# Optimization experiments

Measured on AMD Instinct MI355X. Metric: run time of the kernel, lower is better.

The kernel has to match this reference:

```python
import jax, jax.numpy as jnp
import numpy as np

EMBED_DIM = 1024
NUM_HEADS = 16
HEAD_DIM = EMBED_DIM // NUM_HEADS
ROPE_BASE = 10000.0


def setup_inputs() -> dict:
    key = jax.random.key(0)
    ks = jax.random.split(key, 9)
    B, S, E = 2, 2048, EMBED_DIM
    scale = 1.0 / np.sqrt(E)
    x = jax.random.normal(ks[0], (B, S, E), dtype=jnp.float32)
    Wq = jax.random.normal(ks[1], (E, E), dtype=jnp.float32) * scale
    bq = jnp.zeros((E,), dtype=jnp.float32)
    Wk = jax.random.normal(ks[2], (E, E), dtype=jnp.float32) * scale
    bk = jnp.zeros((E,), dtype=jnp.float32)
    Wv = jax.random.normal(ks[3], (E, E), dtype=jnp.float32) * scale
    bv = jnp.zeros((E,), dtype=jnp.float32)
    Wo = jax.random.normal(ks[4], (E, E), dtype=jnp.float32) * scale
    bo = jnp.zeros((E,), dtype=jnp.float32)
    return {"x": x, "Wq": Wq, "bq": bq, "Wk": Wk, "bk": bk,
            "Wv": Wv, "bv": bv, "Wo": Wo, "bo": bo}


def _rotary_emb(seq_len, dtype=jnp.float32):
    half = HEAD_DIM // 2
    inv_freq = 1.0 / (ROPE_BASE ** (jnp.arange(half, dtype=dtype) / half))
    pos = jnp.arange(seq_len, dtype=dtype)
    sinusoid = pos[:, None] * inv_freq[None, :]  # [S, half]
    sin = jnp.sin(sinusoid)
    cos = jnp.cos(sinusoid)
    # interleave-duplicate: (s0,s0,s1,s1,...) -> [S, HEAD_DIM]
    sin = jnp.stack((sin, sin), axis=-1).reshape(seq_len, HEAD_DIM)
    cos = jnp.stack((cos, cos), axis=-1).reshape(seq_len, HEAD_DIM)
    return sin, cos


def _rotate_half(x):
    x1 = x[..., ::2]
    x2 = x[..., 1::2]
    return jnp.stack((-x2, x1), axis=-1).reshape(x.shape)


def _apply_rope(x, sin, cos):
    # x: [B, H, S, D]; sin/cos: [S, D]
    return x * cos[None, None] + _rotate_half(x) * sin[None, None]


def reference(x, Wq, bq, Wk, bk, Wv, bv, Wo, bo):
    B, S, E = x.shape
    H, D = NUM_HEADS, HEAD_DIM

    def proj(W, b):
        t = x @ W.T + b  # [B, S, E]
        return t.reshape(B, S, H, D).transpose(0, 2, 1, 3)  # [B, H, S, D]

    q = proj(Wq, bq)
    k = proj(Wk, bk)
    v = proj(Wv, bv)

    sin, cos = _rotary_emb(S, x.dtype)
    q = _apply_rope(q, sin, cos)
    k = _apply_rope(k, sin, cos)

    scores = jnp.einsum("bhqd,bhkd->bhqk", q, k) / jnp.sqrt(jnp.asarray(D, x.dtype))
    causal = jnp.tril(jnp.ones((S, S), dtype=bool))  # keep lower triangle
    scores = jnp.where(causal[None, None], scores, -jnp.inf)
    weights = jax.nn.softmax(scores, axis=-1)
    out = jnp.einsum("bhqk,bhkd->bhqd", weights, v)
    out = out.transpose(0, 2, 1, 3).reshape(B, S, E)
    return out @ Wo.T + bo
```

## Files before the change

### kernel.cpp

```cpp
#include <hip/hip_runtime.h>
#include <hip/hip_bf16.h>
#include <cstdint>
#include <cstddef>

typedef __hip_bfloat16 bf16;
typedef __attribute__((ext_vector_type(8))) short bf16x8;
typedef __attribute__((ext_vector_type(4))) float f32x4;

#define AS1C(p) ((const __attribute__((address_space(1))) void*)(p))
#define AS3(p)  ((__attribute__((address_space(3))) void*)(p))

constexpr int B_ = 2, S_ = 2048, E_ = 1024, H_ = 16, D_ = 64;
constexpr int M_ = B_ * S_;
constexpr float QSCALE_ = 0.125f * 1.44269504088896340736f;

__device__ __forceinline__ void gload_lds16(const bf16* g, bf16* l) {
  __builtin_amdgcn_global_load_lds(AS1C(g), AS3(l), 16, 0, 0);
}

__device__ __forceinline__ void cast4(const float* __restrict__ in, bf16* __restrict__ out, int i) {
  float4 v = reinterpret_cast<const float4*>(in)[i];
  union { bf16 b[4]; short4 s; } u;
  u.b[0] = __float2bfloat16(v.x);
  u.b[1] = __float2bfloat16(v.y);
  u.b[2] = __float2bfloat16(v.z);
  u.b[3] = __float2bfloat16(v.w);
  reinterpret_cast<short4*>(out)[i] = u.s;
}

__global__ void prep_kernel(const float* __restrict__ x,
                            const float* __restrict__ Wq, const float* __restrict__ Wk,
                            const float* __restrict__ Wv, const float* __restrict__ Wo,
                            const float* __restrict__ bq, const float* __restrict__ bk,
                            const float* __restrict__ bv,
                            bf16* __restrict__ xb, bf16* __restrict__ Wqkvb,
                            bf16* __restrict__ Wob, float* __restrict__ bqkv,
                            float* __restrict__ sintab, float* __restrict__ costab) {
  const int b = blockIdx.x, t = threadIdx.x;
  if (b < 4096) {
    cast4(x, xb, b * 256 + t);
  } else if (b < 5120) {
    cast4(Wo, Wob, (b - 4096) * 256 + t);
  } else if (b < 8192) {
    const int i = (b - 5120) * 256 + t;
    const int which = i >> 18;
    const int j = i & ((1 << 18) - 1);
    const float* src = which == 0 ? Wq : (which == 1 ? Wk : Wv);
    cast4(src, Wqkvb + (size_t)which * E_ * E_, j);
  } else if (b < 8448) {
    const int idx = (b - 8192) * 256 + t;
    const int s = idx >> 5, i = idx & 31;
    float inv = powf(10000.0f, -(float)i / 32.0f);
    float ang = (float)s * inv;
    sintab[idx] = sinf(ang);
    costab[idx] = cosf(ang);
  } else {
    for (int j = t; j < 768; j += 256) {
      const int which = j >> 8, jj = j & 255;
      const float* src = which == 0 ? bq : (which == 1 ? bk : bv);
      reinterpret_cast<float4*>(bqkv)[j] = reinterpret_cast<const float4*>(src)[jj];
    }
  }
}

__global__ __launch_bounds__(256)
void gemm_qkv(const bf16* __restrict__ A, const bf16* __restrict__ W,
              const float* __restrict__ bias,
              bf16* __restrict__ Qo, bf16* __restrict__ Ko, bf16* __restrict__ Vo,
              const float* __restrict__ sintab, const float* __restrict__ costab)
{
  constexpr int K = 1024, BK = 32;
  __shared__ __align__(16) bf16 smem[128 * 136];
  bf16* As = smem;
  bf16* Bs = smem + 128 * 32;
  const int tid = threadIdx.x;
  const int lane = tid & 63, wid = tid >> 6;
  const int g = lane >> 4, r16 = lane & 15;
  const int wr = wid >> 1, wc = wid & 1;

  const int nwg = gridDim.x * gridDim.y;
  const int flat = blockIdx.y * gridDim.x + blockIdx.x;
  const int cpx = nwg >> 3;
  const int f2 = (flat & 7) * cpx + (flat >> 3);
  const int m0 = (f2 / gridDim.x) * 128, n0 = (f2 % gridDim.x) * 128;

  const f32x4 fz = {0.f, 0.f, 0.f, 0.f};
  f32x4 acc[4][4];
#pragma unroll
  for (int mi = 0; mi < 4; ++mi)
#pragma unroll
    for (int ni = 0; ni < 4; ++ni) acc[mi][ni] = fz;

  const bf16* Abase = A + (size_t)m0 * K;
  const bf16* Wbase = W + (size_t)n0 * K;
  const int c0 = tid, c1 = 256 + tid;

  for (int k0 = 0; k0 < K; k0 += BK) {
    __syncthreads();
    gload_lds16(Abase + (size_t)(c0 >> 2) * K + k0 + (c0 & 3) * 8, As + c0 * 8);
    gload_lds16(Abase + (size_t)(c1 >> 2) * K + k0 + (c1 & 3) * 8, As + c1 * 8);
    gload_lds16(Wbase + (size_t)(c0 >> 2) * K + k0 + (c0 & 3) * 8, Bs + c0 * 8);
    gload_lds16(Wbase + (size_t)(c1 >> 2) * K + k0 + (c1 & 3) * 8, Bs + c1 * 8);
    __syncthreads();

    bf16x8 af[4], bfr[4];
#pragma unroll
    for (int mi = 0; mi < 4; ++mi)
      af[mi] = *reinterpret_cast<const bf16x8*>(As + (wr * 64 + mi * 16 + r16) * BK + 8 * g);
#pragma unroll
    for (int ni = 0; ni < 4; ++ni)
      bfr[ni] = *reinterpret_cast<const bf16x8*>(Bs + (wc * 64 + ni * 16 + r16) * BK + 8 * g);
    __builtin_amdgcn_s_setprio(1);
#pragma unroll
    for (int mi = 0; mi < 4; ++mi)
#pragma unroll
      for (int ni = 0; ni < 4; ++ni)
        acc[mi][ni] = __builtin_amdgcn_mfma_f32_16x16x32_bf16(af[mi], bfr[ni], acc[mi][ni], 0, 0, 0);
    __builtin_amdgcn_s_setprio(0);
  }

  const int b = m0 >> 11;
  if (n0 >= 2048) {
    __syncthreads();
#pragma unroll
    for (int mi = 0; mi < 4; ++mi) {
#pragma unroll
      for (int ni = 0; ni < 4; ++ni) {
        const int n_local = wc * 64 + ni * 16 + r16;
        const float bv = bias[n0 + n_local];
        const int m_base = wr * 64 + mi * 16 + g * 4;
        union { bf16 b4[4]; short4 s4; } u;
#pragma unroll
        for (int r = 0; r < 4; ++r) u.b4[r] = __float2bfloat16(acc[mi][ni][r] + bv);
        *reinterpret_cast<short4*>(&smem[n_local * 136 + m_base]) = u.s4;
      }
    }
    __syncthreads();
    const int srow0 = m0 & (S_ - 1);
#pragma unroll
    for (int i = 0; i < 8; ++i) {
      const int c = i * 256 + tid;
      const int row = c >> 4, cc = c & 15;
      const bf16x8 v = *reinterpret_cast<const bf16x8*>(&smem[row * 136 + cc * 8]);
      const int n = n0 + row;
      const int h = (n >> 6) & 15, d = n & 63;
      *reinterpret_cast<bf16x8*>(&Vo[((size_t)(b * H_ + h) * D_ + d) * S_ + srow0 + cc * 8]) = v;
    }
  } else {
#pragma unroll
    for (int mi = 0; mi < 4; ++mi) {
#pragma unroll
      for (int ni = 0; ni < 4; ++ni) {
        const int gn = n0 + wc * 64 + ni * 16 + r16;
        const float bv = bias[gn];
#pragma unroll
        for (int r = 0; r < 4; ++r) {
          const int gm = m0 + wr * 64 + mi * 16 + g * 4 + r;
          float val = acc[mi][ni][r] + bv;
          const int d = gn & 63;
          const int srow = gm & (S_ - 1);
          const float cs = costab[srow * 32 + (d >> 1)];
          const float sn = sintab[srow * 32 + (d >> 1)];
          const float pv = __shfl_xor(val, 1);
          val = (d & 1) ? (val * cs + pv * sn) : (val * cs - pv * sn);
          const int h = (gn >> 6) & 15;
          const size_t bh = (size_t)(b * H_ + h);
          if (gn < 1024) {
            Qo[(bh * S_ + srow) * D_ + d] = __float2bfloat16(val * QSCALE_);
          } else {
            Ko[(bh * S_ + srow) * D_ + d] = __float2bfloat16(val);
          }
        }
      }
    }
  }
}

__global__ __launch_bounds__(256)
void gemm_o(const bf16* __restrict__ A, const bf16* __restrict__ W,
            const float* __restrict__ bias, float* __restrict__ outF)
{
  constexpr int K = 1024, BK = 32;
  __shared__ __align__(16) bf16 As[64 * BK];
  __shared__ __align__(16) bf16 Bs[128 * BK];
  const int tid = threadIdx.x;
  const int lane = tid & 63;
  const int wc = tid >> 6;
  const int g = lane >> 4, r16 = lane & 15;

  const int flat = blockIdx.x;
  const int f2 = (flat & 7) * 64 + (flat >> 3);
  const int m0 = (f2 >> 3) * 64, n0 = (f2 & 7) * 128;

  const f32x4 fz = {0.f, 0.f, 0.f, 0.f};
  f32x4 acc[4][2];
#pragma unroll
  for (int mi = 0; mi < 4; ++mi)
#pragma unroll
    for (int ni = 0; ni < 2; ++ni) acc[mi][ni] = fz;

  const bf16* Abase = A + (size_t)m0 * K;
  const bf16* Wbase = W + (size_t)n0 * K;
  const int c0 = tid, c1 = 256 + tid;

  for (int k0 = 0; k0 < K; k0 += BK) {
    __syncthreads();
    gload_lds16(Abase + (size_t)(c0 >> 2) * K + k0 + (c0 & 3) * 8, As + c0 * 8);
    gload_lds16(Wbase + (size_t)(c0 >> 2) * K + k0 + (c0 & 3) * 8, Bs + c0 * 8);
    gload_lds16(Wbase + (size_t)(c1 >> 2) * K + k0 + (c1 & 3) * 8, Bs + c1 * 8);
    __syncthreads();

    bf16x8 af[4], bfr[2];
#pragma unroll
    for (int mi = 0; mi < 4; ++mi)
      af[mi] = *reinterpret_cast<const bf16x8*>(As + (mi * 16 + r16) * BK + 8 * g);
#pragma unroll
    for (int ni = 0; ni < 2; ++ni)
      bfr[ni] = *reinterpret_cast<const bf16x8*>(Bs + (wc * 32 + ni * 16 + r16) * BK + 8 * g);
    __builtin_amdgcn_s_setprio(1);
#pragma unroll
    for (int mi = 0; mi < 4; ++mi)
#pragma unroll
      for (int ni = 0; ni < 2; ++ni)
        acc[mi][ni] = __builtin_amdgcn_mfma_f32_16x16x32_bf16(af[mi], bfr[ni], acc[mi][ni], 0, 0, 0);
    __builtin_amdgcn_s_setprio(0);
  }

#pragma unroll
  for (int mi = 0; mi < 4; ++mi)
#pragma unroll
    for (int ni = 0; ni < 2; ++ni) {
      const int gn = n0 + wc * 32 + ni * 16 + r16;
      const float bv = bias[gn];
#pragma unroll
      for (int r = 0; r < 4; ++r) {
        const int gm = m0 + mi * 16 + g * 4 + r;
        outF[(size_t)gm * 1024 + gn] = acc[mi][ni][r] + bv;
      }
    }
}

__global__ __launch_bounds__(256, 4)
void attn_kernel(const bf16* __restrict__ Q, const bf16* __restrict__ Kg,
                 const bf16* __restrict__ Vtg, bf16* __restrict__ Og)
{
  __shared__ __align__(16) bf16 Ks[2][64 * 64];
  __shared__ __align__(16) bf16 Vs[2][64 * 64];
  const int flat = blockIdx.x;
  const int bh = flat & 31;
  const int qblk = 31 - (flat >> 5);
  const int tid = threadIdx.x, lane = tid & 63, wid = tid >> 6;
  const int g = lane >> 4, r16 = lane & 15;
  const bf16* Qb = Q + (size_t)bh * S_ * D_;
  const bf16* Kb = Kg + (size_t)bh * S_ * D_;
  const bf16* Vb = Vtg + (size_t)bh * D_ * S_;
  const int b = bh >> 4, h = bh & 15;
  bf16* Ob = Og + (size_t)b * S_ * E_ + h * D_;

  const int q0 = qblk * 64;
  const int qw0 = q0 + wid * 16;
  const int nkt = qblk + 1;
  const f32x4 fz = {0.f, 0.f, 0.f, 0.f};

  bf16x8 qf[2];
#pragma unroll
  for (int hh = 0; hh < 2; ++hh)
    qf[hh] = *reinterpret_cast<const bf16x8*>(Qb + (size_t)(qw0 + r16) * 64 + hh * 32 + 8 * g);

  f32x4 oacc[4];
#pragma unroll
  for (int dt = 0; dt < 4; ++dt) oacc[dt] = fz;
  float mrow = -__builtin_inff();
  float lrow = 0.f;

  const int kc0 = tid, kc1 = 256 + tid;
  const int glsrc = (g << 4) + (g << 2);

  auto stage = [&](const bf16* srcbase, size_t rowstride, bf16* dst) {
    const int r0 = kc0 >> 3, cc0 = kc0 & 7;
    gload_lds16(srcbase + (size_t)r0 * rowstride + ((cc0 ^ (r0 & 7)) * 8), dst + kc0 * 8);
    const int r1 = kc1 >> 3, cc1 = kc1 & 7;
    gload_lds16(srcbase + (size_t)r1 * rowstride + ((cc1 ^ (r1 & 7)) * 8), dst + kc1 * 8);
  };

  stage(Kb, 64, Ks[0]);
  stage(Vb, S_, Vs[0]);
  __syncthreads();
  int cur = 0;

  for (int kt = 0; kt < nkt; ++kt) {
    const int k0 = kt * 64;
    if (kt + 1 < nkt) {
      stage(Kb + (size_t)(k0 + 64) * 64, 64, Ks[cur ^ 1]);
      stage(Vb + (k0 + 64), S_, Vs[cur ^ 1]);
    }

    if (k0 <= qw0 + 15) {
      const bf16* ksp = Ks[cur];
      const bf16* vsp = Vs[cur];
      const int sw = r16 & 7;
      f32x4 ps[4];
      __builtin_amdgcn_s_setprio(1);
#pragma unroll
      for (int kf = 0; kf < 4; ++kf) {
        const int krow = kf * 16 + r16;
        const bf16x8 ka = *reinterpret_cast<const bf16x8*>(&ksp[krow * 64 + ((g ^ sw) * 8)]);
        const bf16x8 kb = *reinterpret_cast<const bf16x8*>(&ksp[krow * 64 + (((g + 4) ^ sw) * 8)]);
        f32x4 sa = __builtin_amdgcn_mfma_f32_16x16x32_bf16(ka, qf[0], fz, 0, 0, 0);
        ps[kf] = __builtin_amdgcn_mfma_f32_16x16x32_bf16(kb, qf[1], sa, 0, 0, 0);
      }
      __builtin_amdgcn_s_setprio(0);
      if (k0 + 63 > qw0) {
        const int qmk = qw0 + r16 - k0;
#pragma unroll
        for (int kf = 0; kf < 4; ++kf)
#pragma unroll
          for (int r = 0; r < 4; ++r)
            if (kf * 16 + 4 * g + r > qmk) ps[kf][r] = -1e30f;
      }
      float tm = fmaxf(fmaxf(ps[0][0], ps[0][1]), fmaxf(ps[0][2], ps[0][3]));
#pragma unroll
      for (int kf = 1; kf < 4; ++kf)
        tm = fmaxf(tm, fmaxf(fmaxf(ps[kf][0], ps[kf][1]), fmaxf(ps[kf][2], ps[kf][3])));
      tm = fmaxf(tm, __shfl_xor(tm, 16));
      tm = fmaxf(tm, __shfl_xor(tm, 32));
      if (__any((tm - mrow > 8.f) ? 1 : 0)) {
        const float mn = fmaxf(mrow, tm);
        const float scl = exp2f(mrow - mn);
        mrow = mn;
        lrow *= scl;
        float sclo[4];
#pragma unroll
        for (int r = 0; r < 4; ++r) sclo[r] = __shfl(scl, glsrc + r);
#pragma unroll
        for (int dt = 0; dt < 4; ++dt)
#pragma unroll
          for (int r = 0; r < 4; ++r) oacc[dt][r] *= sclo[r];
      }
      float ssum = 0.f;
#pragma unroll
      for (int kf = 0; kf < 4; ++kf)
#pragma unroll
        for (int r = 0; r < 4; ++r) {
          const float p = exp2f(ps[kf][r] - mrow);
          ps[kf][r] = p;
          ssum += p;
        }
      lrow += ssum;
      unsigned int pk[4][2];
#pragma unroll
      for (int kf = 0; kf < 4; ++kf)
#pragma unroll
        for (int w = 0; w < 2; ++w) {
          unsigned int rr;
          asm("v_cvt_pk_bf16_f32 %0, %1, %2" : "=v"(rr) : "v"(ps[kf][2 * w]), "v"(ps[kf][2 * w + 1]));
          pk[kf][w] = rr;
        }
      const int srcA = ((g & 1) << 5) + r16;
      const bool ghi = g >= 2;
#pragma unroll
      for (int ks = 0; ks < 2; ++ks) {
        const unsigned int a0 = (unsigned)__shfl((int)pk[2 * ks][0], srcA);
        const unsigned int b0 = (unsigned)__shfl((int)pk[2 * ks + 1][0], srcA);
        const unsigned int a1 = (unsigned)__shfl((int)pk[2 * ks][1], srcA);
        const unsigned int b1 = (unsigned)__shfl((int)pk[2 * ks + 1][1], srcA);
        const unsigned int a2 = (unsigned)__shfl((int)pk[2 * ks][0], srcA + 16);
        const unsigned int b2 = (unsigned)__shfl((int)pk[2 * ks + 1][0], srcA + 16);
        const unsigned int a3 = (unsigned)__shfl((int)pk[2 * ks][1], srcA + 16);
        const unsigned int b3 = (unsigned)__shfl((int)pk[2 * ks + 1][1], srcA + 16);
        union { unsigned int w[4]; bf16x8 v; } aw;
        aw.w[0] = ghi ? b0 : a0;
        aw.w[1] = ghi ? b1 : a1;
        aw.w[2] = ghi ? b2 : a2;
        aw.w[3] = ghi ? b3 : a3;
        __builtin_amdgcn_s_setprio(1);
#pragma unroll
        for (int dt = 0; dt < 4; ++dt) {
          const int d = dt * 16 + r16;
          const bf16x8 vf = *reinterpret_cast<const bf16x8*>(
              &vsp[d * 64 + (((ks * 4 + g) ^ (r16 & 7)) * 8)]);
          oacc[dt] = __builtin_amdgcn_mfma_f32_16x16x32_bf16(aw.v, vf, oacc[dt], 0, 0, 0);
        }
        __builtin_amdgcn_s_setprio(0);
      }
    }

    __syncthreads();
    cur ^= 1;
  }

  float s = lrow;
  s += __shfl_xor(s, 16);
  s += __shfl_xor(s, 32);
  const float linv = 1.0f / s;
  float linvo[4];
#pragma unroll
  for (int r = 0; r < 4; ++r) linvo[r] = __shfl(linv, glsrc + r);
#pragma unroll
  for (int dt = 0; dt < 4; ++dt)
#pragma unroll
    for (int r = 0; r < 4; ++r) {
      const int qrow = qw0 + g * 4 + r;
      Ob[(size_t)qrow * E_ + dt * 16 + r16] = __float2bfloat16(oacc[dt][r] * linvo[r]);
    }
}

extern "C" void kernel_launch(void* const* d_in, const int* in_sizes, int n_in,
                              void* d_out, int out_size, void* d_ws, size_t ws_size,
                              hipStream_t stream) {
  const float* x  = (const float*)d_in[0];
  const float* Wq = (const float*)d_in[1];
  const float* bq = (const float*)d_in[2];
  const float* Wk = (const float*)d_in[3];
  const float* bk = (const float*)d_in[4];
  const float* Wv = (const float*)d_in[5];
  const float* bv = (const float*)d_in[6];
  const float* Wo = (const float*)d_in[7];
  const float* bo = (const float*)d_in[8];
  float* out = (float*)d_out;

  char* ws = (char*)d_ws;
  size_t off = 0;
  auto alloc = [&](size_t bytes) -> char* {
    char* p = ws + off; off += (bytes + 255) & ~(size_t)255; return p;
  };
  bf16* xb    = (bf16*)alloc((size_t)M_ * E_ * 2);
  bf16* Wqkvb = (bf16*)alloc((size_t)3 * E_ * E_ * 2);
  bf16* Wob   = (bf16*)alloc((size_t)E_ * E_ * 2);
  float* bqkv = (float*)alloc((size_t)3 * E_ * 4);
  bf16* Qb    = (bf16*)alloc((size_t)M_ * E_ * 2);
  bf16* Kb    = (bf16*)alloc((size_t)M_ * E_ * 2);
  bf16* Vtb   = (bf16*)alloc((size_t)M_ * E_ * 2);
  bf16* AOb   = (bf16*)alloc((size_t)M_ * E_ * 2);
  float* sintab = (float*)alloc((size_t)S_ * 32 * 4);
  float* costab = (float*)alloc((size_t)S_ * 32 * 4);

  prep_kernel<<<dim3(8449), 256, 0, stream>>>(x, Wq, Wk, Wv, Wo, bq, bk, bv,
                                              xb, Wqkvb, Wob, bqkv, sintab, costab);

  gemm_qkv<<<dim3(24, 32), 256, 0, stream>>>(xb, Wqkvb, bqkv, Qb, Kb, Vtb, sintab, costab);
  attn_kernel<<<dim3(1024), 256, 0, stream>>>(Qb, Kb, Vtb, AOb);
  gemm_o<<<dim3(512), 256, 0, stream>>>(AOb, Wob, bo, out);
}
```

Before: 135.0 us.

## Switch attention to 32x32x16 MFMA with 128-row query blocks

Rewrites the attention inner loop to use 32x32x16 bf16 MFMA tiles. Each wave now owns 32 query rows and a block covers 128 queries, so every staged K/V tile is reused by twice as many query rows and the grid is halved. The P-matrix relayout now uses v_permlane32_swap instead of many shuffles. The risks are higher register pressure, since the launch-bounds occupancy hint was dropped, and fewer blocks to balance the causal workload across CUs.

```diff
diff --git a/kernel.cpp b/kernel.cpp
--- a/kernel.cpp
+++ b/kernel.cpp
@@ -6,6 +6,7 @@
 typedef __hip_bfloat16 bf16;
 typedef __attribute__((ext_vector_type(8))) short bf16x8;
 typedef __attribute__((ext_vector_type(4))) float f32x4;
+typedef __attribute__((ext_vector_type(16))) float f32x16;
 
 #define AS1C(p) ((const __attribute__((address_space(1))) void*)(p))
 #define AS3(p)  ((__attribute__((address_space(3))) void*)(p))
@@ -240,7 +241,7 @@
     }
 }
 
-__global__ __launch_bounds__(256, 4)
+__global__ __launch_bounds__(256)
 void attn_kernel(const bf16* __restrict__ Q, const bf16* __restrict__ Kg,
                  const bf16* __restrict__ Vtg, bf16* __restrict__ Og)
 {
@@ -248,34 +249,30 @@
   __shared__ __align__(16) bf16 Vs[2][64 * 64];
   const int flat = blockIdx.x;
   const int bh = flat & 31;
-  const int qblk = 31 - (flat >> 5);
+  const int qblk = 15 - (flat >> 5);
   const int tid = threadIdx.x, lane = tid & 63, wid = tid >> 6;
-  const int g = lane >> 4, r16 = lane & 15;
+  const int l31 = lane & 31, h = lane >> 5;
   const bf16* Qb = Q + (size_t)bh * S_ * D_;
   const bf16* Kb = Kg + (size_t)bh * S_ * D_;
   const bf16* Vb = Vtg + (size_t)bh * D_ * S_;
-  const int b = bh >> 4, h = bh & 15;
-  bf16* Ob = Og + (size_t)b * S_ * E_ + h * D_;
-
-  const int q0 = qblk * 64;
-  const int qw0 = q0 + wid * 16;
-  const int nkt = qblk + 1;
-  const f32x4 fz = {0.f, 0.f, 0.f, 0.f};
-
-  bf16x8 qf[2];
-#pragma unroll
-  for (int hh = 0; hh < 2; ++hh)
-    qf[hh] = *reinterpret_cast<const bf16x8*>(Qb + (size_t)(qw0 + r16) * 64 + hh * 32 + 8 * g);
-
-  f32x4 oacc[4];
-#pragma unroll
-  for (int dt = 0; dt < 4; ++dt) oacc[dt] = fz;
+  const int b = bh >> 4, hd = bh & 15;
+  bf16* Ob = Og + (size_t)b * S_ * E_ + hd * D_;
+
+  const int q0 = qblk * 128;
+  const int qw0 = q0 + wid * 32;
+  const int nkt = 2 * qblk + 2;
+
+  bf16x8 qf[4];
+#pragma unroll
+  for (int i = 0; i < 4; ++i)
+    qf[i] = *reinterpret_cast<const bf16x8*>(Qb + (size_t)(qw0 + l31) * 64 + 16 * i + 8 * h);
+
+  f32x16 oacc0 = {};
+  f32x16 oacc1 = {};
   float mrow = -__builtin_inff();
   float lrow = 0.f;
 
   const int kc0 = tid, kc1 = 256 + tid;
-  const int glsrc = (g << 4) + (g << 2);
-
   auto stage = [&](const bf16* srcbase, size_t rowstride, bf16* dst) {
     const int r0 = kc0 >> 3, cc0 = kc0 & 7;
     gload_lds16(srcbase + (size_t)r0 * rowstride + ((cc0 ^ (r0 & 7)) * 8), dst + kc0 * 8);
@@ -295,92 +292,93 @@
       stage(Vb + (k0 + 64), S_, Vs[cur ^ 1]);
     }
 
-    if (k0 <= qw0 + 15) {
+    if (k0 <= qw0 + 31) {
       const bf16* ksp = Ks[cur];
       const bf16* vsp = Vs[cur];
-      const int sw = r16 & 7;
-      f32x4 ps[4];
+      f32x16 ps0 = {}, ps1 = {};
       __builtin_amdgcn_s_setprio(1);
 #pragma unroll
-      for (int kf = 0; kf < 4; ++kf) {
-        const int krow = kf * 16 + r16;
-        const bf16x8 ka = *reinterpret_cast<const bf16x8*>(&ksp[krow * 64 + ((g ^ sw) * 8)]);
-        const bf16x8 kb = *reinterpret_cast<const bf16x8*>(&ksp[krow * 64 + (((g + 4) ^ sw) * 8)]);
-        f32x4 sa = __builtin_amdgcn_mfma_f32_16x16x32_bf16(ka, qf[0], fz, 0, 0, 0);
-        ps[kf] = __builtin_amdgcn_mfma_f32_16x16x32_bf16(kb, qf[1], sa, 0, 0, 0);
+      for (int i = 0; i < 4; ++i) {
+        const int row0 = l31;
+        const bf16x8 ka0 = *reinterpret_cast<const bf16x8*>(
+            &ksp[row0 * 64 + (((2 * i + h) ^ (row0 & 7)) * 8)]);
+        ps0 = __builtin_amdgcn_mfma_f32_32x32x16_bf16(ka0, qf[i], ps0, 0, 0, 0);
+      }
+#pragma unroll
+      for (int i = 0; i < 4; ++i) {
+        const int row1 = 32 + l31;
+        const bf16x8 ka1 = *reinterpret_cast<const bf16x8*>(
+            &ksp[row1 * 64 + (((2 * i + h) ^ (row1 & 7)) * 8)]);
+        ps1 = __builtin_amdgcn_mfma_f32_32x32x16_bf16(ka1, qf[i], ps1, 0, 0, 0);
       }
       __builtin_amdgcn_s_setprio(0);
       if (k0 + 63 > qw0) {
-        const int qmk = qw0 + r16 - k0;
-#pragma unroll
-        for (int kf = 0; kf < 4; ++kf)
-#pragma unroll
-          for (int r = 0; r < 4; ++r)
-            if (kf * 16 + 4 * g + r > qmk) ps[kf][r] = -1e30f;
-      }
-      float tm = fmaxf(fmaxf(ps[0][0], ps[0][1]), fmaxf(ps[0][2], ps[0][3]));
-#pragma unroll
-      for (int kf = 1; kf < 4; ++kf)
-        tm = fmaxf(tm, fmaxf(fmaxf(ps[kf][0], ps[kf][1]), fmaxf(ps[kf][2], ps[kf][3])));
-      tm = fmaxf(tm, __shfl_xor(tm, 16));
+        const int qm = qw0 + l31 - k0;
+#pragma unroll
+        for (int r = 0; r < 16; ++r) {
+          const int kl = (r & 3) + 8 * (r >> 2) + 4 * h;
+          if (kl > qm) ps0[r] = -1e30f;
+          if (32 + kl > qm) ps1[r] = -1e30f;
+        }
+      }
+      float tm = ps0[0];
+#pragma unroll
+      for (int r = 1; r < 16; ++r) tm = fmaxf(tm, ps0[r]);
+#pragma unroll
+      for (int r = 0; r < 16; ++r) tm = fmaxf(tm, ps1[r]);
       tm = fmaxf(tm, __shfl_xor(tm, 32));
       if (__any((tm - mrow > 8.f) ? 1 : 0)) {
         const float mn = fmaxf(mrow, tm);
         const float scl = exp2f(mrow - mn);
         mrow = mn;
         lrow *= scl;
-        float sclo[4];
-#pragma unroll
-        for (int r = 0; r < 4; ++r) sclo[r] = __shfl(scl, glsrc + r);
-#pragma unroll
-        for (int dt = 0; dt < 4; ++dt)
-#pragma unroll
-          for (int r = 0; r < 4; ++r) oacc[dt][r] *= sclo[r];
+        float so[16];
+#pragma unroll
+        for (int r = 0; r < 16; ++r)
+          so[r] = __shfl(scl, (r & 3) + 8 * (r >> 2) + 4 * h);
+#pragma unroll
+        for (int r = 0; r < 16; ++r) { oacc0[r] *= so[r]; oacc1[r] *= so[r]; }
       }
       float ssum = 0.f;
 #pragma unroll
-      for (int kf = 0; kf < 4; ++kf)
-#pragma unroll
-        for (int r = 0; r < 4; ++r) {
-          const float p = exp2f(ps[kf][r] - mrow);
-          ps[kf][r] = p;
-          ssum += p;
-        }
+      for (int r = 0; r < 16; ++r) {
+        const float p = exp2f(ps0[r] - mrow);
+        ps0[r] = p; ssum += p;
+      }
+#pragma unroll
+      for (int r = 0; r < 16; ++r) {
+        const float p = exp2f(ps1[r] - mrow);
+        ps1[r] = p; ssum += p;
+      }
       lrow += ssum;
-      unsigned int pk[4][2];
-#pragma unroll
-      for (int kf = 0; kf < 4; ++kf)
-#pragma unroll
-        for (int w = 0; w < 2; ++w) {
-          unsigned int rr;
-          asm("v_cvt_pk_bf16_f32 %0, %1, %2" : "=v"(rr) : "v"(ps[kf][2 * w]), "v"(ps[kf][2 * w + 1]));
-          pk[kf][w] = rr;
-        }
-      const int srcA = ((g & 1) << 5) + r16;
-      const bool ghi = g >= 2;
-#pragma unroll
-      for (int ks = 0; ks < 2; ++ks) {
-        const unsigned int a0 = (unsigned)__shfl((int)pk[2 * ks][0], srcA);
-        const unsigned int b0 = (unsigned)__shfl((int)pk[2 * ks + 1][0], srcA);
-        const unsigned int a1 = (unsigned)__shfl((int)pk[2 * ks][1], srcA);
-        const unsigned int b1 = (unsigned)__shfl((int)pk[2 * ks + 1][1], srcA);
-        const unsigned int a2 = (unsigned)__shfl((int)pk[2 * ks][0], srcA + 16);
-        const unsigned int b2 = (unsigned)__shfl((int)pk[2 * ks + 1][0], srcA + 16);
-        const unsigned int a3 = (unsigned)__shfl((int)pk[2 * ks][1], srcA + 16);
-        const unsigned int b3 = (unsigned)__shfl((int)pk[2 * ks + 1][1], srcA + 16);
-        union { unsigned int w[4]; bf16x8 v; } aw;
-        aw.w[0] = ghi ? b0 : a0;
-        aw.w[1] = ghi ? b1 : a1;
-        aw.w[2] = ghi ? b2 : a2;
-        aw.w[3] = ghi ? b3 : a3;
+      unsigned int pk0[8], pk1[8];
+#pragma unroll
+      for (int i = 0; i < 8; ++i) {
+        unsigned int r0, r1;
+        asm("v_cvt_pk_bf16_f32 %0, %1, %2" : "=v"(r0) : "v"(ps0[2 * i]), "v"(ps0[2 * i + 1]));
+        asm("v_cvt_pk_bf16_f32 %0, %1, %2" : "=v"(r1) : "v"(ps1[2 * i]), "v"(ps1[2 * i + 1]));
+        pk0[i] = r0; pk1[i] = r1;
+      }
+#pragma unroll
+      for (int ks = 0; ks < 4; ++ks) {
+        const int ksl = ks & 1;
+        unsigned int w0, w1, w2, w3;
+        if (ks < 2) { w0 = pk0[4 * ksl]; w2 = pk0[4 * ksl + 2];
+                      w1 = pk0[4 * ksl + 1]; w3 = pk0[4 * ksl + 3]; }
+        else        { w0 = pk1[4 * ksl]; w2 = pk1[4 * ksl + 2];
+                      w1 = pk1[4 * ksl + 1]; w3 = pk1[4 * ksl + 3]; }
+        asm("v_permlane32_swap_b32 %0, %1" : "+v"(w0), "+v"(w2));
+        asm("v_permlane32_swap_b32 %0, %1" : "+v"(w1), "+v"(w3));
+        union { unsigned int w[4]; bf16x8 v; } A;
+        A.w[0] = w0; A.w[1] = w1; A.w[2] = w2; A.w[3] = w3;
+        const int sw = l31 & 7;
+        const bf16x8 vf0 = *reinterpret_cast<const bf16x8*>(
+            &vsp[l31 * 64 + (((2 * ks + h) ^ sw) * 8)]);
+        const bf16x8 vf1 = *reinterpret_cast<const bf16x8*>(
+            &vsp[(32 + l31) * 64 + (((2 * ks + h) ^ sw) * 8)]);
         __builtin_amdgcn_s_setprio(1);
-#pragma unroll
-        for (int dt = 0; dt < 4; ++dt) {
-          const int d = dt * 16 + r16;
-          const bf16x8 vf = *reinterpret_cast<const bf16x8*>(
-              &vsp[d * 64 + (((ks * 4 + g) ^ (r16 & 7)) * 8)]);
-          oacc[dt] = __builtin_amdgcn_mfma_f32_16x16x32_bf16(aw.v, vf, oacc[dt], 0, 0, 0);
-        }
+        oacc0 = __builtin_amdgcn_mfma_f32_32x32x16_bf16(A.v, vf0, oacc0, 0, 0, 0);
+        oacc1 = __builtin_amdgcn_mfma_f32_32x32x16_bf16(A.v, vf1, oacc1, 0, 0, 0);
         __builtin_amdgcn_s_setprio(0);
       }
     }
@@ -389,20 +387,18 @@
     cur ^= 1;
   }
 
-  float s = lrow;
-  s += __shfl_xor(s, 16);
-  s += __shfl_xor(s, 32);
+  float s = lrow + __shfl_xor(lrow, 32);
   const float linv = 1.0f / s;
-  float linvo[4];
-#pragma unroll
-  for (int r = 0; r < 4; ++r) linvo[r] = __shfl(linv, glsrc + r);
-#pragma unroll
-  for (int dt = 0; dt < 4; ++dt)
-#pragma unroll
-    for (int r = 0; r < 4; ++r) {
-      const int qrow = qw0 + g * 4 + r;
-      Ob[(size_t)qrow * E_ + dt * 16 + r16] = __float2bfloat16(oacc[dt][r] * linvo[r]);
-    }
+  float lo[16];
+#pragma unroll
+  for (int r = 0; r < 16; ++r)
+    lo[r] = __shfl(linv, (r & 3) + 8 * (r >> 2) + 4 * h);
+#pragma unroll
+  for (int r = 0; r < 16; ++r) {
+    const int qrow = qw0 + (r & 3) + 8 * (r >> 2) + 4 * h;
+    Ob[(size_t)qrow * E_ + l31] = __float2bfloat16(oacc0[r] * lo[r]);
+    Ob[(size_t)qrow * E_ + 32 + l31] = __float2bfloat16(oacc1[r] * lo[r]);
+  }
 }
 
 extern "C" void kernel_launch(void* const* d_in, const int* in_sizes, int n_in,
@@ -439,6 +435,6 @@
                                               xb, Wqkvb, Wob, bqkv, sintab, costab);
 
   gemm_qkv<<<dim3(24, 32), 256, 0, stream>>>(xb, Wqkvb, bqkv, Qb, Kb, Vtb, sintab, costab);
-  attn_kernel<<<dim3(1024), 256, 0, stream>>>(Qb, Kb, Vtb, AOb);
+  attn_kernel<<<dim3(512), 256, 0, stream>>>(Qb, Kb, Vtb, AOb);
   gemm_o<<<dim3(512), 256, 0, stream>>>(AOb, Wob, bo, out);
 }
```

Result: slower. 143.8 us (+6.5%).
